# Performance work log

Measured on AMD Instinct MI355X. Metric: run time of the kernel, lower is better.

## Reference

```python
import jax, jax.numpy as jnp
import numpy as np

S = 8            # n_internal_streams
N = 2**S - 1     # 255 cliques (all non-empty subsets of streams)
D = 32           # half_dim = consciousness_dim // 2
INPUT_DIM = 512
NUM_ITER = 5
B = 1024


def _configs():
    # binary membership of each clique (non-empty subsets), [N, S]
    return ((np.arange(1, 2**S)[:, None] >> np.arange(S)) & 1).astype(np.float32)


def setup_inputs() -> dict:
    key = jax.random.key(0)
    ks = jax.random.split(key, 10)
    cfg = _configs()
    depths = cfg.sum(-1)
    # topological amplitude init: gaussian profile over clique depth
    center, sigma = S / 2.0, S / 3.0
    prof = np.exp(-((depths - center) ** 2) / (2 * sigma ** 2))
    prof = prof / (np.linalg.norm(prof) + 1e-8)
    psi_A0 = jnp.asarray(np.broadcast_to(prof[None, :, None], (1, N, D)).copy(),
                         jnp.float32) + jax.random.normal(ks[0], (1, N, D)) * 0.01
    inp = {
        'network_state': jax.random.normal(ks[1], (B, INPUT_DIM), jnp.float32),
        'W_streams': jax.random.normal(ks[2], (S * D, INPUT_DIM)) / np.sqrt(INPUT_DIM),
        'b_streams': jnp.zeros((S * D,), jnp.float32),
        'W_A': jax.random.normal(ks[3], (D, D)) / np.sqrt(D),
        'b_A': jnp.zeros((D,), jnp.float32),
        'W_phi': jax.random.normal(ks[4], (D, D)) / np.sqrt(D),
        'b_phi': jnp.zeros((D,), jnp.float32),
        'psi_A0': psi_A0,
        'psi_phi0': jax.random.normal(ks[5], (1, N, D)) * 0.3,
        'W_comp': jax.random.normal(ks[6], (32, N)) / np.sqrt(N),
        'b_comp': jnp.zeros((32,), jnp.float32),
        'W_read': jax.random.normal(ks[7], (2 * D, 32 * D)) / np.sqrt(32 * D),
        'b_read': jnp.zeros((2 * D,), jnp.float32),
        'alpha_kin': jnp.asarray(0.5, jnp.float32),
        'mass_sq': jnp.asarray(0.1, jnp.float32),
        'potential_weight': jnp.asarray(0.3, jnp.float32),
        'input_weight': jnp.asarray(0.5, jnp.float32),
        'evolution_rate': jnp.asarray(0.3, jnp.float32),
        'phase_coupling': jnp.asarray(1.0, jnp.float32),
    }
    return inp


def reference(network_state, W_streams, b_streams, W_A, b_A, W_phi, b_phi,
              psi_A0, psi_phi0, W_comp, b_comp, W_read, b_read,
              alpha_kin, mass_sq, potential_weight, input_weight,
              evolution_rate, phase_coupling):
    cfg = jnp.asarray(_configs())                      # [N,S]
    depths = cfg.sum(-1)                               # [N]
    # Hamming-distance kernel between clique configurations
    Ham = cfg @ (1.0 - cfg).T + (1.0 - cfg) @ cfg.T    # [N,N]
    K = jnp.exp(-Ham / S)
    krow = K.sum(1)                                    # [N]

    Bb = network_state.shape[0]
    feats = (network_state @ W_streams.T + b_streams).reshape(Bb, S, D)
    # clique features: mean of member-stream features
    cf = jnp.einsum('ns,bsd->bnd', cfg, feats) / depths[None, :, None]
    A_input = jax.nn.softplus(cf @ W_A.T + b_A)        # [B,N,D]
    phi_input = jnp.pi * jnp.tanh(cf @ W_phi.T + b_phi)

    A = jax.nn.softplus(jnp.broadcast_to(psi_A0, (Bb, N, D)))
    phi = jnp.broadcast_to(psi_phi0, (Bb, N, D))
    dt = jax.nn.sigmoid(evolution_rate)

    for _ in range(NUM_ITER):
        # laplacian: sum_j K_ij (A_j - A_i) / N  (factorized, same math)
        KA = jnp.einsum('ij,bjd->bid', K, A)
        lap = (KA - krow[None, :, None] * A) / N
        sp, cp = jnp.sin(phi), jnp.cos(phi)
        Ks = jnp.einsum('ij,bjd->bid', K, sp)
        Kc = jnp.einsum('ij,bjd->bid', K, cp)
        # sum_j K_ij A_i sin(phi_j - phi_i) / N
        pc = A * (cp * Ks - sp * Kc) / N
        # nonlocal potential: V_i = sum_j K_ij A_j cos(phi_j - phi_i) / N
        KAc = jnp.einsum('ij,bjd->bid', K, A * cp)
        KAs = jnp.einsum('ij,bjd->bid', K, A * sp)
        V = (cp * KAc + sp * KAs) / N
        input_drive = A_input * jnp.sin(phi_input - phi)
        dA = (alpha_kin * lap + potential_weight * V - mass_sq * A
              + input_weight * (A_input - A))
        A = jax.nn.softplus(A + dt * dA)               # updated A used in dphi
        dphi = alpha_kin * pc / (A + 1e-8) + input_weight * input_drive
        phi = phi + dt * dphi
        # per-clique norm clip to 1
        norms = jnp.maximum(jnp.linalg.norm(A, axis=-1, keepdims=True), 1e-8)
        A = A * jnp.where(norms > 1.0, 1.0 / norms, 1.0)

    A_t = jnp.swapaxes(A, 1, 2)                        # [B,D,N]
    Ac = jax.nn.relu(A_t @ W_comp.T + b_comp)          # [B,D,32]
    ro = Ac.reshape(Bb, -1) @ W_read.T + b_read        # [B,2D]
    amplitude = jax.nn.softplus(ro[:, :D])
    phase = jnp.tanh(ro[:, D:] * phase_coupling) * jnp.pi
    psi = (amplitude * jnp.cos(phase)).astype(jnp.complex64) + 1j * (amplitude * jnp.sin(phase)).astype(jnp.complex64)
    return psi, amplitude, phase
```

## Files before the change

### kernel.cpp

```cpp
#include <hip/hip_runtime.h>
#include <math.h>

#define PI_F   3.14159265358979f
#define QF     0.88249690258459546f
#define INV255 (1.0f/255.0f)

__device__ __forceinline__ float softplus_f(float x){
    return fmaxf(x, 0.0f) + __logf(1.0f + __expf(-fabsf(x)));
}
__device__ __forceinline__ float tanh_fast(float x){
    const float e = __expf(2.0f*x);
    return fmaf(-2.0f, __builtin_amdgcn_rcpf(e + 1.0f), 1.0f);
}

template<int CTRL>
__device__ __forceinline__ float dppmov(float x){
    return __int_as_float(__builtin_amdgcn_mov_dpp(__float_as_int(x), CTRL, 0xF, 0xF, false));
}
__device__ __forceinline__ float lxor1 (float x){ return dppmov<0xB1>(x);  }
__device__ __forceinline__ float lxor2 (float x){ return dppmov<0x4E>(x);  }
__device__ __forceinline__ float lxor8 (float x){ return dppmov<0x128>(x); }
__device__ __forceinline__ float lxor4 (float x){ return __int_as_float(__builtin_amdgcn_ds_swizzle(__float_as_int(x), 0x101F)); }
__device__ __forceinline__ float lxor16(float x){ return __int_as_float(__builtin_amdgcn_ds_swizzle(__float_as_int(x), 0x401F)); }
__device__ __forceinline__ float lxor32(float x){ return __shfl_xor(x, 32, 64); }

template<int CTRL>
__device__ __forceinline__ float dppadd(float v){
    return v + __int_as_float(__builtin_amdgcn_update_dpp(0, __float_as_int(v), CTRL, 0xF, 0xF, true));
}
__device__ __forceinline__ float wave_sum63(float v){
    v = dppadd<0x111>(v);
    v = dppadd<0x112>(v);
    v = dppadd<0x114>(v);
    v = dppadd<0x118>(v);
    v = dppadd<0x142>(v);
    v = dppadd<0x143>(v);
    return v;
}

__device__ __forceinline__ void bfly20(float (&x)[5][4]){
    const float qv = QF;
    #pragma unroll
    for (int a = 0; a < 5; a++){
        #pragma unroll
        for (int r = 0; r < 4; r++) x[a][r] = fmaf(lxor1 (x[a][r]), qv, x[a][r]);
    }
    #pragma unroll
    for (int a = 0; a < 5; a++){
        #pragma unroll
        for (int r = 0; r < 4; r++) x[a][r] = fmaf(lxor2 (x[a][r]), qv, x[a][r]);
    }
    #pragma unroll
    for (int a = 0; a < 5; a++){
        #pragma unroll
        for (int r = 0; r < 4; r++) x[a][r] = fmaf(lxor8 (x[a][r]), qv, x[a][r]);
    }
    #pragma unroll
    for (int a = 0; a < 5; a++){
        #pragma unroll
        for (int r = 0; r < 4; r++) x[a][r] = fmaf(lxor4 (x[a][r]), qv, x[a][r]);
    }
    #pragma unroll
    for (int a = 0; a < 5; a++){
        #pragma unroll
        for (int r = 0; r < 4; r++) x[a][r] = fmaf(lxor16(x[a][r]), qv, x[a][r]);
    }
    #pragma unroll
    for (int a = 0; a < 5; a++){
        #pragma unroll
        for (int r = 0; r < 4; r++) x[a][r] = fmaf(lxor32(x[a][r]), qv, x[a][r]);
    }
    #pragma unroll
    for (int a = 0; a < 5; a++){
        float t0 = x[a][0], t2 = x[a][2];
        x[a][0] = fmaf(QF, x[a][1], x[a][0]);
        x[a][1] = fmaf(QF, t0,      x[a][1]);
        x[a][2] = fmaf(QF, x[a][3], x[a][2]);
        x[a][3] = fmaf(QF, t2,      x[a][3]);
        t0 = x[a][0]; float t1 = x[a][1];
        x[a][0] = fmaf(QF, x[a][2], x[a][0]);
        x[a][1] = fmaf(QF, x[a][3], x[a][1]);
        x[a][2] = fmaf(QF, t0,      x[a][2]);
        x[a][3] = fmaf(QF, t1,      x[a][3]);
    }
}

__global__ __launch_bounds__(256) void transpose_ws(
        const float* __restrict__ Ws, float* __restrict__ WsT)
{
    __shared__ float tile[64][65];
    const int rt = blockIdx.x & 3, ct = blockIdx.x >> 2;
    const int r0 = rt*64, c0 = ct*64;
    const int tx = threadIdx.x & 63, ty = threadIdx.x >> 6;
    #pragma unroll
    for (int k = 0; k < 16; k++){
        const int row = ty*16 + k;
        tile[row][tx] = Ws[(r0+row)*512 + c0 + tx];
    }
    __syncthreads();
    #pragma unroll
    for (int k = 0; k < 16; k++){
        const int row = ty*16 + k;
        WsT[(c0+row)*256 + r0 + tx] = tile[tx][row];
    }
}

template<bool USET>
__global__ __launch_bounds__(256) void fused_kernel(
        const float* __restrict__ ns,
        const float* __restrict__ Ws,
        const float* __restrict__ WsT,
        const float* __restrict__ bs,
        const float* __restrict__ WA,
        const float* __restrict__ bA,
        const float* __restrict__ WP,
        const float* __restrict__ bP,
        const float* __restrict__ psiA0,
        const float* __restrict__ psiP0,
        const float* __restrict__ Wcomp,
        const float* __restrict__ bcomp,
        const float* __restrict__ Wread,
        const float* __restrict__ bread,
        const float* __restrict__ p_alpha, const float* __restrict__ p_msq,
        const float* __restrict__ p_pw,    const float* __restrict__ p_iw,
        const float* __restrict__ p_evo,   const float* __restrict__ p_pcpl,
        float* __restrict__ out, int Bb)
{
    __shared__ __align__(16) float nsb[512];
    __shared__ __align__(16) float fe[256];
    __shared__ __align__(16) float hA[256];
    __shared__ __align__(16) float hP[256];
    __shared__ __align__(16) float red[2][1024];
    __shared__ __align__(16) float ac[1024];
    __shared__ __align__(16) float rop[256];

    const int b   = blockIdx.x;
    const int tid = threadIdx.x;
    const int w   = tid >> 6, l = tid & 63;

    const float alpha = p_alpha[0], msq = p_msq[0], pw = p_pw[0], iw = p_iw[0];
    const float pcpl  = p_pcpl[0];
    const float dt    = 1.0f / (1.0f + __expf(-p_evo[0]));
    const float dta  = dt * alpha * INV255;
    const float dtpw = dt * pw * INV255;
    const float c0   = 1.0f - dt * (msq + iw);
    const float dtiw = dt * iw;

    nsb[tid]       = ns[b*512 + tid];
    nsb[tid + 256] = ns[b*512 + 256 + tid];
    __syncthreads();
    if (USET){
        float f = bs[tid];
        const float4* nb4 = (const float4*)nsb;
        #pragma unroll 8
        for (int j4 = 0; j4 < 128; j4++){
            const float4 nv = nb4[j4];
            const float* col = WsT + j4*1024 + tid;
            f = fmaf(col[0],   nv.x, f);
            f = fmaf(col[256], nv.y, f);
            f = fmaf(col[512], nv.z, f);
            f = fmaf(col[768], nv.w, f);
        }
        fe[tid] = f;
    } else {
        float f = bs[tid];
        const float4* wr  = (const float4*)(Ws + tid*512);
        const float4* nb4 = (const float4*)nsb;
        #pragma unroll 8
        for (int i = 0; i < 128; i++){
            const float4 wv = wr[i], nv = nb4[i];
            f = fmaf(wv.x, nv.x, f); f = fmaf(wv.y, nv.y, f);
            f = fmaf(wv.z, nv.z, f); f = fmaf(wv.w, nv.w, f);
        }
        fe[tid] = f;
    }
    __syncthreads();
    {
        const int s = tid >> 5, d = tid & 31;
        float a = 0.0f, p = 0.0f;
        #pragma unroll 8
        for (int dp = 0; dp < 32; dp++){
            const float fv = fe[s*32 + dp];
            a = fmaf(WA[d*32 + dp], fv, a);
            p = fmaf(WP[d*32 + dp], fv, p);
        }
        hA[tid] = a; hP[tid] = p;
    }
    __syncthreads();

    int   nn[4];
    float krow[4], rdep[4];
    const float m0 = (l == 0) ? 0.0f : 1.0f;
    float c18;
    { const float t1 = 1.0f + QF, t2 = t1*t1, t4 = t2*t2; c18 = t4*t4; }
    #pragma unroll
    for (int r = 0; r < 4; r++){
        nn[r] = l + 64*r;
        const int pop = __popc(nn[r]);
        krow[r]  = c18 - __expf(-0.125f * (float)pop);
        rdep[r]  = 1.0f / (float)(pop ? pop : 1);
    }

    float A[8][4], phi[8][4], CAp[8][4], Dsp[8][4], Dcp[8][4];

    #pragma unroll
    for (int dd = 0; dd < 8; dd++){
        const int d = w*8 + dd;
        const float bAd = bA[d], bPd = bP[d];
        float gA_[8], gP_[8];
        #pragma unroll
        for (int s = 0; s < 8; s++){ gA_[s] = hA[s*32 + d]; gP_[s] = hP[s*32 + d]; }
        #pragma unroll
        for (int r = 0; r < 4; r++){
            float sA = 0.0f, sP = 0.0f;
            #pragma unroll
            for (int s = 0; s < 8; s++){
                if ((nn[r] >> s) & 1){ sA += gA_[s]; sP += gP_[s]; }
            }
            const float uA  = fmaf(sA, rdep[r], bAd);
            const float uP  = fmaf(sP, rdep[r], bPd);
            const float Ain = softplus_f(uA);
            const float pin = PI_F * tanh_fast(uP);
            float si, ci; __sincosf(pin, &si, &ci);
            const float ca = dtiw * Ain;
            CAp[dd][r] = ca; Dsp[dd][r] = ca * si; Dcp[dd][r] = ca * ci;
            const int nm1 = (nn[r] > 0) ? (nn[r] - 1) : 0;
            A[dd][r]   = softplus_f(psiA0[nm1*32 + d]);
            phi[dd][r] = psiP0[nm1*32 + d];
        }
    }

    for (int it = 0; it < 5; it++){
        const int pbuf = it & 1;
        float nrm[4] = {0.f, 0.f, 0.f, 0.f};
        #pragma unroll
        for (int dd = 0; dd < 8; dd++){
            float sp[4], cp[4];
            float x[5][4];
            {
                __sincosf(phi[dd][0], &sp[0], &cp[0]);
                const float xa = A[dd][0] * m0;
                x[0][0] = xa;
                x[1][0] = sp[0] * m0;
                x[2][0] = cp[0] * m0;
                x[3][0] = xa * cp[0];
                x[4][0] = xa * sp[0];
            }
            #pragma unroll
            for (int r = 1; r < 4; r++){
                __sincosf(phi[dd][r], &sp[r], &cp[r]);
                const float xa = A[dd][r];
                x[0][r] = xa;
                x[1][r] = sp[r];
                x[2][r] = cp[r];
                x[3][r] = xa * cp[r];
                x[4][r] = xa * sp[r];
            }
            bfly20(x);
            #pragma unroll
            for (int r = 0; r < 4; r++){
                const float Ao   = A[dd][r];
                const float lapp = fmaf(-krow[r], Ao, x[0][r]);
                const float Vp   = fmaf(cp[r], x[3][r], sp[r]*x[4][r]);
                float Aarg = fmaf(c0, Ao, CAp[dd][r]);
                Aarg = fmaf(dta,  lapp, Aarg);
                Aarg = fmaf(dtpw, Vp,   Aarg);
                const float An = softplus_f(Aarg);
                const float Pp = fmaf(-sp[r], x[2][r], cp[r]*x[1][r]);
                const float rr = __builtin_amdgcn_rcpf(An + 1e-8f);
                float pb = fmaf(Dsp[dd][r], cp[r], phi[dd][r]);
                pb = fmaf(-Dcp[dd][r], sp[r], pb);
                phi[dd][r] = fmaf(dta*Ao, Pp*rr, pb);
                A[dd][r]   = An;
                nrm[r]     = fmaf(An, An, nrm[r]);
            }
        }
        #pragma unroll
        for (int r = 0; r < 4; r++) red[pbuf][w*256 + nn[r]] = nrm[r];
        __syncthreads();
        float scl[4];
        #pragma unroll
        for (int r = 0; r < 4; r++){
            const float t = red[pbuf][nn[r]] + red[pbuf][256 + nn[r]]
                          + red[pbuf][512 + nn[r]] + red[pbuf][768 + nn[r]];
            scl[r] = (t > 1.0f) ? rsqrtf(t) : 1.0f;
        }
        #pragma unroll
        for (int dd = 0; dd < 8; dd++)
            #pragma unroll
            for (int r = 0; r < 4; r++) A[dd][r] *= scl[r];
    }

    #pragma unroll
    for (int dd = 0; dd < 8; dd++) A[dd][0] *= m0;

    for (int c = 0; c < 32; c++){
        float wv[4];
        #pragma unroll
        for (int r = 0; r < 4; r++){
            const int idx = c*255 + nn[r] - 1;
            wv[r] = Wcomp[idx < 0 ? 0 : idx];
        }
        const float bc = bcomp[c];
        #pragma unroll
        for (int dd = 0; dd < 8; dd++){
            float v = wv[0] * A[dd][0];
            v = fmaf(wv[1], A[dd][1], v);
            v = fmaf(wv[2], A[dd][2], v);
            v = fmaf(wv[3], A[dd][3], v);
            v = wave_sum63(v);
            if (l == 63)
                ac[(w*8 + dd)*32 + c] = fmaxf(v + bc, 0.0f);
        }
    }
    __syncthreads();

    {
        const int k = tid >> 2, part = tid & 3;
        const float4* Wr4 = (const float4*)Wread + k*256;
        const float4* ac4 = (const float4*)ac;
        float s = 0.0f;
        #pragma unroll 4
        for (int jj = 0; jj < 64; jj++){
            const int j4 = part + 4*jj;
            const float4 wv = Wr4[j4];
            const float4 av = ac4[j4];
            s = fmaf(wv.x, av.x, s); s = fmaf(wv.y, av.y, s);
            s = fmaf(wv.z, av.z, s); s = fmaf(wv.w, av.w, s);
        }
        rop[tid] = s;
    }
    __syncthreads();
    if (tid < 32){
        const float ra = rop[tid*4] + rop[tid*4+1] + rop[tid*4+2] + rop[tid*4+3] + bread[tid];
        const int   t2 = tid + 32;
        const float rp = rop[t2*4] + rop[t2*4+1] + rop[t2*4+2] + rop[t2*4+3] + bread[t2];
        const float amp = softplus_f(ra);
        const float ph  = PI_F * tanhf(rp * pcpl);
        const float cph = __cosf(ph);
        const int o = b*32 + tid;
        out[o]         = amp * cph;
        out[Bb*32 + o] = amp;
        out[Bb*64 + o] = ph;
    }
}

extern "C" void kernel_launch(void* const* d_in, const int* in_sizes, int n_in,
                              void* d_out, int out_size, void* d_ws, size_t ws_size,
                              hipStream_t stream) {
    const float* ns      = (const float*)d_in[0];
    const float* Ws      = (const float*)d_in[1];
    const float* bs      = (const float*)d_in[2];
    const float* WA      = (const float*)d_in[3];
    const float* bA      = (const float*)d_in[4];
    const float* WP      = (const float*)d_in[5];
    const float* bP      = (const float*)d_in[6];
    const float* psiA0   = (const float*)d_in[7];
    const float* psiP0   = (const float*)d_in[8];
    const float* Wcomp   = (const float*)d_in[9];
    const float* bcomp   = (const float*)d_in[10];
    const float* Wread   = (const float*)d_in[11];
    const float* bread   = (const float*)d_in[12];
    const float* p_alpha = (const float*)d_in[13];
    const float* p_msq   = (const float*)d_in[14];
    const float* p_pw    = (const float*)d_in[15];
    const float* p_iw    = (const float*)d_in[16];
    const float* p_evo   = (const float*)d_in[17];
    const float* p_pcpl  = (const float*)d_in[18];

    const int Bb = in_sizes[0] / 512;

    if (ws_size >= (size_t)(512*256*sizeof(float))){
        float* WsT = (float*)d_ws;
        transpose_ws<<<32, 256, 0, stream>>>(Ws, WsT);
        fused_kernel<true><<<Bb, 256, 0, stream>>>(ns, Ws, WsT, bs, WA, bA, WP, bP,
                                                   psiA0, psiP0, Wcomp, bcomp,
                                                   Wread, bread, p_alpha, p_msq, p_pw, p_iw,
                                                   p_evo, p_pcpl, (float*)d_out, Bb);
    } else {
        fused_kernel<false><<<Bb, 256, 0, stream>>>(ns, Ws, nullptr, bs, WA, bA, WP, bP,
                                                    psiA0, psiP0, Wcomp, bcomp,
                                                    Wread, bread, p_alpha, p_msq, p_pw, p_iw,
                                                    p_evo, p_pcpl, (float*)d_out, Bb);
    }
}
```

Before: 335.2 us.

## Double block size to 512 threads, halving per-wave dimension work

Launches the fused kernel with 512 threads (8 waves) instead of 256. Each wave now owns 4 of the 32 feature dimensions instead of 8, which halves the per-thread register arrays. The input projection is split into two K-halves with a shared-memory partial reduction, and the readout dot products use 8 partial sums per output. The aim is to cut register pressure and per-thread serial latency so each block finishes sooner. The cost is more shared memory, extra barriers and a longer cross-wave reduction for the norm clip.

```diff
diff --git a/kernel.cpp b/kernel.cpp
--- a/kernel.cpp
+++ b/kernel.cpp
@@ -106,7 +106,7 @@
 }
 
 template<bool USET>
-__global__ __launch_bounds__(256) void fused_kernel(
+__global__ __launch_bounds__(512) void fused_kernel(
         const float* __restrict__ ns,
         const float* __restrict__ Ws,
         const float* __restrict__ WsT,
@@ -127,12 +127,13 @@
         float* __restrict__ out, int Bb)
 {
     __shared__ __align__(16) float nsb[512];
+    __shared__ __align__(16) float pfe[512];
     __shared__ __align__(16) float fe[256];
     __shared__ __align__(16) float hA[256];
     __shared__ __align__(16) float hP[256];
-    __shared__ __align__(16) float red[2][1024];
+    __shared__ __align__(16) float red[2][2048];
     __shared__ __align__(16) float ac[1024];
-    __shared__ __align__(16) float rop[256];
+    __shared__ __align__(16) float rop[512];
 
     const int b   = blockIdx.x;
     const int tid = threadIdx.x;
@@ -146,36 +147,38 @@
     const float c0   = 1.0f - dt * (msq + iw);
     const float dtiw = dt * iw;
 
-    nsb[tid]       = ns[b*512 + tid];
-    nsb[tid + 256] = ns[b*512 + 256 + tid];
-    __syncthreads();
-    if (USET){
-        float f = bs[tid];
-        const float4* nb4 = (const float4*)nsb;
-        #pragma unroll 8
-        for (int j4 = 0; j4 < 128; j4++){
-            const float4 nv = nb4[j4];
-            const float* col = WsT + j4*1024 + tid;
-            f = fmaf(col[0],   nv.x, f);
-            f = fmaf(col[256], nv.y, f);
-            f = fmaf(col[512], nv.z, f);
-            f = fmaf(col[768], nv.w, f);
-        }
-        fe[tid] = f;
-    } else {
-        float f = bs[tid];
-        const float4* wr  = (const float4*)(Ws + tid*512);
-        const float4* nb4 = (const float4*)nsb;
-        #pragma unroll 8
-        for (int i = 0; i < 128; i++){
-            const float4 wv = wr[i], nv = nb4[i];
-            f = fmaf(wv.x, nv.x, f); f = fmaf(wv.y, nv.y, f);
-            f = fmaf(wv.z, nv.z, f); f = fmaf(wv.w, nv.w, f);
-        }
-        fe[tid] = f;
-    }
+    nsb[tid] = ns[b*512 + tid];
     __syncthreads();
     {
+        const int ff = tid & 255, half = tid >> 8;
+        float f = half ? 0.0f : bs[ff];
+        const float4* nb4 = (const float4*)nsb + half*64;
+        if (USET){
+            const float* base = WsT + (half*256)*256 + ff;
+            #pragma unroll 8
+            for (int j4 = 0; j4 < 64; j4++){
+                const float4 nv = nb4[j4];
+                const float* col = base + j4*1024;
+                f = fmaf(col[0],   nv.x, f);
+                f = fmaf(col[256], nv.y, f);
+                f = fmaf(col[512], nv.z, f);
+                f = fmaf(col[768], nv.w, f);
+            }
+        } else {
+            const float4* wr = (const float4*)(Ws + ff*512) + half*64;
+            #pragma unroll 8
+            for (int i = 0; i < 64; i++){
+                const float4 wv = wr[i], nv = nb4[i];
+                f = fmaf(wv.x, nv.x, f); f = fmaf(wv.y, nv.y, f);
+                f = fmaf(wv.z, nv.z, f); f = fmaf(wv.w, nv.w, f);
+            }
+        }
+        pfe[tid] = f;
+    }
+    __syncthreads();
+    if (tid < 256) fe[tid] = pfe[tid] + pfe[tid + 256];
+    __syncthreads();
+    if (tid < 256){
         const int s = tid >> 5, d = tid & 31;
         float a = 0.0f, p = 0.0f;
         #pragma unroll 8
@@ -201,11 +204,11 @@
         rdep[r]  = 1.0f / (float)(pop ? pop : 1);
     }
 
-    float A[8][4], phi[8][4], CAp[8][4], Dsp[8][4], Dcp[8][4];
-
-    #pragma unroll
-    for (int dd = 0; dd < 8; dd++){
-        const int d = w*8 + dd;
+    float A[4][4], phi[4][4], CAp[4][4], Dsp[4][4], Dcp[4][4];
+
+    #pragma unroll
+    for (int dd = 0; dd < 4; dd++){
+        const int d = w*4 + dd;
         const float bAd = bA[d], bPd = bP[d];
         float gA_[8], gP_[8];
         #pragma unroll
@@ -234,7 +237,7 @@
         const int pbuf = it & 1;
         float nrm[4] = {0.f, 0.f, 0.f, 0.f};
         #pragma unroll
-        for (int dd = 0; dd < 8; dd++){
+        for (int dd = 0; dd < 4; dd++){
             float sp[4], cp[4];
             float x[5][4];
             {
@@ -281,18 +284,19 @@
         float scl[4];
         #pragma unroll
         for (int r = 0; r < 4; r++){
-            const float t = red[pbuf][nn[r]] + red[pbuf][256 + nn[r]]
-                          + red[pbuf][512 + nn[r]] + red[pbuf][768 + nn[r]];
+            float t = 0.0f;
+            #pragma unroll
+            for (int wp = 0; wp < 8; wp++) t += red[pbuf][wp*256 + nn[r]];
             scl[r] = (t > 1.0f) ? rsqrtf(t) : 1.0f;
         }
         #pragma unroll
-        for (int dd = 0; dd < 8; dd++)
+        for (int dd = 0; dd < 4; dd++)
             #pragma unroll
             for (int r = 0; r < 4; r++) A[dd][r] *= scl[r];
     }
 
     #pragma unroll
-    for (int dd = 0; dd < 8; dd++) A[dd][0] *= m0;
+    for (int dd = 0; dd < 4; dd++) A[dd][0] *= m0;
 
     for (int c = 0; c < 32; c++){
         float wv[4];
@@ -303,26 +307,26 @@
         }
         const float bc = bcomp[c];
         #pragma unroll
-        for (int dd = 0; dd < 8; dd++){
+        for (int dd = 0; dd < 4; dd++){
             float v = wv[0] * A[dd][0];
             v = fmaf(wv[1], A[dd][1], v);
             v = fmaf(wv[2], A[dd][2], v);
             v = fmaf(wv[3], A[dd][3], v);
             v = wave_sum63(v);
             if (l == 63)
-                ac[(w*8 + dd)*32 + c] = fmaxf(v + bc, 0.0f);
+                ac[(w*4 + dd)*32 + c] = fmaxf(v + bc, 0.0f);
         }
     }
     __syncthreads();
 
     {
-        const int k = tid >> 2, part = tid & 3;
+        const int k = tid >> 3, part = tid & 7;
         const float4* Wr4 = (const float4*)Wread + k*256;
         const float4* ac4 = (const float4*)ac;
         float s = 0.0f;
         #pragma unroll 4
-        for (int jj = 0; jj < 64; jj++){
-            const int j4 = part + 4*jj;
+        for (int jj = 0; jj < 32; jj++){
+            const int j4 = part + 8*jj;
             const float4 wv = Wr4[j4];
             const float4 av = ac4[j4];
             s = fmaf(wv.x, av.x, s); s = fmaf(wv.y, av.y, s);
@@ -332,9 +336,12 @@
     }
     __syncthreads();
     if (tid < 32){
-        const float ra = rop[tid*4] + rop[tid*4+1] + rop[tid*4+2] + rop[tid*4+3] + bread[tid];
-        const int   t2 = tid + 32;
-        const float rp = rop[t2*4] + rop[t2*4+1] + rop[t2*4+2] + rop[t2*4+3] + bread[t2];
+        float ra = bread[tid], rp = bread[tid + 32];
+        #pragma unroll
+        for (int p = 0; p < 8; p++){
+            ra += rop[tid*8 + p];
+            rp += rop[(tid + 32)*8 + p];
+        }
         const float amp = softplus_f(ra);
         const float ph  = PI_F * tanhf(rp * pcpl);
         const float cph = __cosf(ph);
@@ -373,12 +380,12 @@
     if (ws_size >= (size_t)(512*256*sizeof(float))){
         float* WsT = (float*)d_ws;
         transpose_ws<<<32, 256, 0, stream>>>(Ws, WsT);
-        fused_kernel<true><<<Bb, 256, 0, stream>>>(ns, Ws, WsT, bs, WA, bA, WP, bP,
+        fused_kernel<true><<<Bb, 512, 0, stream>>>(ns, Ws, WsT, bs, WA, bA, WP, bP,
                                                    psiA0, psiP0, Wcomp, bcomp,
                                                    Wread, bread, p_alpha, p_msq, p_pw, p_iw,
                                                    p_evo, p_pcpl, (float*)d_out, Bb);
     } else {
-        fused_kernel<false><<<Bb, 256, 0, stream>>>(ns, Ws, nullptr, bs, WA, bA, WP, bP,
+        fused_kernel<false><<<Bb, 512, 0, stream>>>(ns, Ws, nullptr, bs, WA, bA, WP, bP,
                                                     psiA0, psiP0, Wcomp, bcomp,
                                                     Wread, bread, p_alpha, p_msq, p_pw, p_iw,
                                                     p_evo, p_pcpl, (float*)d_out, Bb);
```

After: 362.0 us. +8.0%, slower.
